# Optimization experiments

Hardware: AMD Instinct MI355X
Metric: run time of the kernel (lower is better)

The kernel has to match this reference:

```python
import jax, jax.numpy as jnp
import numpy as np

N_NODES = 100000
N_EDGES = 1600000
N_GRAPHS = 512
IN_F, H1, H2 = 128, 128, 256
N_GROUPS, N_FAM = 16, 10


def setup_inputs() -> dict:
    key = jax.random.key(0)
    ks = jax.random.split(key, 8)
    x = jax.random.normal(ks[0], (N_NODES, IN_F), dtype=jnp.float32)
    edge_index = jax.random.randint(ks[1], (2, N_EDGES), 0, N_NODES, dtype=jnp.int64)
    batch = jnp.sort(jax.random.randint(ks[2], (N_NODES,), 0, N_GRAPHS, dtype=jnp.int64))
    W1 = jax.random.normal(ks[3], (IN_F, H1), dtype=jnp.float32) / np.sqrt(IN_F)
    b1 = jnp.zeros((H1,), dtype=jnp.float32)
    W2 = jax.random.normal(ks[4], (H1, H2), dtype=jnp.float32) / np.sqrt(H1)
    b2 = jnp.zeros((H2,), dtype=jnp.float32)
    Wg = jax.random.normal(ks[5], (H2, N_GROUPS), dtype=jnp.float32) / np.sqrt(H2)
    bg = jnp.zeros((N_GROUPS,), dtype=jnp.float32)
    Wf = jax.random.normal(ks[6], (N_GROUPS, H2, N_FAM), dtype=jnp.float32) / np.sqrt(H2)
    bf = jnp.zeros((N_GROUPS, N_FAM), dtype=jnp.float32)
    return {"x": x, "edge_index": edge_index, "batch": batch,
            "W1": W1, "b1": b1, "W2": W2, "b2": b2,
            "Wg": Wg, "bg": bg, "Wf": Wf, "bf": bf}


def gcn_conv(x, W, b, src, dst, num_nodes):
    # PyG GCNConv: add self-loops, symmetric normalization, scatter-add aggregation.
    xw = x @ W  # [N, out]
    deg = jax.ops.segment_sum(jnp.ones((src.shape[0],), x.dtype), dst,
                              num_segments=num_nodes) + 1.0  # +1 self-loop
    dinv = jax.lax.rsqrt(deg)
    coef = dinv[src] * dinv[dst]            # [E]
    msg = xw[src] * coef[:, None]           # gather + scale (memory-bound)
    agg = jax.ops.segment_sum(msg, dst, num_segments=num_nodes)
    agg = agg + xw * (dinv * dinv)[:, None]  # self-loop contribution
    return agg + b


def reference(x, edge_index, batch, W1, b1, W2, b2, Wg, bg, Wf, bf):
    src, dst = edge_index[0], edge_index[1]
    h = jax.nn.relu(gcn_conv(x, W1, b1, src, dst, N_NODES))
    # dropout p=0.5 is identity in eval mode
    h = gcn_conv(h, W2, b2, src, dst, N_NODES)
    # global mean pool over graphs
    sums = jax.ops.segment_sum(h, batch, num_segments=N_GRAPHS)       # [G, H2]
    cnts = jax.ops.segment_sum(jnp.ones((N_NODES,), h.dtype), batch,
                               num_segments=N_GRAPHS)
    pooled = sums / jnp.maximum(cnts, 1.0)[:, None]
    group_logits = pooled @ Wg + bg                                   # [G, num_groups]
    family_logits = jnp.einsum('bd,gdf->gbf', pooled, Wf) + bf[:, None, :]
    return group_logits, family_logits
```

## Files before the change

kernel.cpp:

```cpp
#include <hip/hip_runtime.h>

#define NN 100000
#define NE 1600000
#define NGR 512
#define KF 128
#define H2F 256
#define NGRP 16
#define NFAM 10

#define CH 128
#define NCHUNK ((NN + CH - 1) / CH)
#define PT 6656
#define NT ((NE + PT - 1) / PT)

typedef __attribute__((ext_vector_type(8))) short short8;
typedef __attribute__((ext_vector_type(4))) float floatx4;

__device__ __forceinline__ unsigned short f2bf(float f) {
  unsigned u = __float_as_uint(f);
  unsigned r = (u + 0x7fff + ((u >> 16) & 1)) >> 16;
  return (unsigned short)r;
}
__device__ __forceinline__ float2 bf2f(unsigned u) {
  float2 r;
  r.x = __uint_as_float(u << 16);
  r.y = __uint_as_float(u & 0xffff0000u);
  return r;
}


__global__ __launch_bounds__(256) void k_phist(const int* __restrict__ ei,
                                               int* __restrict__ mat) {
  __shared__ int lh[NCHUNK];
  int t0 = blockIdx.x, tid = threadIdx.x;
  for (int g = tid; g < NCHUNK; g += 256) lh[g] = 0;
  __syncthreads();
  int base = t0 * PT;
  int nv = min(PT, NE - base);
  for (int i = tid; i < nv; i += 256) atomicAdd(&lh[ei[NE + base + i] >> 7], 1);
  __syncthreads();
  for (int g = tid; g < NCHUNK; g += 256) mat[t0 * NCHUNK + g] = lh[g];
}

__global__ __launch_bounds__(256) void k_colsum(const int* __restrict__ mat,
                                                int* __restrict__ tot) {
  int g = blockIdx.x * 4 + (threadIdx.x >> 6);
  if (g >= NCHUNK) return;
  int lane = threadIdx.x & 63;
  int s = 0;
  for (int t = lane; t < NT; t += 64) s += mat[t * NCHUNK + g];
#pragma unroll
  for (int off = 32; off > 0; off >>= 1) s += __shfl_down(s, off);
  if (lane == 0) tot[g] = s;
}

__global__ __launch_bounds__(256) void k_scantot(const int* __restrict__ tot,
                                                 int* __restrict__ cbase) {
  __shared__ int ssc[256];
  int tid = threadIdx.x;
  int v4[4]; int loc = 0;
#pragma unroll
  for (int j = 0; j < 4; ++j) {
    int idx = tid * 4 + j;
    v4[j] = (idx < NCHUNK) ? tot[idx] : 0;
    loc += v4[j];
  }
  ssc[tid] = loc;
  __syncthreads();
  for (int off = 1; off < 256; off <<= 1) {
    int val = (tid >= off) ? ssc[tid - off] : 0;
    __syncthreads();
    ssc[tid] += val;
    __syncthreads();
  }
  int excl = ssc[tid] - loc;
#pragma unroll
  for (int j = 0; j < 4; ++j) {
    int idx = tid * 4 + j;
    if (idx < NCHUNK) cbase[idx] = excl;
    excl += v4[j];
  }
  if (tid == 255) cbase[NCHUNK] = excl;
}

__global__ __launch_bounds__(256) void k_colfix(int* __restrict__ mat,
                                                const int* __restrict__ cbase) {
  int g = blockIdx.x * 4 + (threadIdx.x >> 6);
  if (g >= NCHUNK) return;
  int lane = threadIdx.x & 63;
  int v[4]; int loc = 0;
#pragma unroll
  for (int j = 0; j < 4; ++j) {
    int t = lane * 4 + j;
    v[j] = (t < NT) ? mat[t * NCHUNK + g] : 0;
    loc += v[j];
  }
  int incl = loc;
#pragma unroll
  for (int off = 1; off < 64; off <<= 1) {
    int o = __shfl_up(incl, off);
    if (lane >= off) incl += o;
  }
  int excl = incl - loc + cbase[g];
#pragma unroll
  for (int j = 0; j < 4; ++j) {
    int t = lane * 4 + j;
    if (t < NT) mat[t * NCHUNK + g] = excl;
    excl += v[j];
  }
}

__global__ __launch_bounds__(256) void k_pscatter(const int* __restrict__ ei,
                                                  const int* __restrict__ mat,
                                                  int2* __restrict__ erec) {
  __shared__ int2 stage[PT];
  __shared__ int lstart[NCHUNK];
  __shared__ int lrun[NCHUNK];
  __shared__ int loff[NCHUNK];
  __shared__ int ssc[256];
  int t0 = blockIdx.x, tid = threadIdx.x;
  for (int g = tid; g < NCHUNK; g += 256) lrun[g] = 0;
  __syncthreads();
  int base = t0 * PT;
  int nv = min(PT, NE - base);
  for (int i = tid; i < nv; i += 256) atomicAdd(&lrun[ei[NE + base + i] >> 7], 1);
  __syncthreads();
  int v4[4]; int loc = 0;
#pragma unroll
  for (int j = 0; j < 4; ++j) {
    int idx = tid * 4 + j;
    v4[j] = (idx < NCHUNK) ? lrun[idx] : 0;
    loc += v4[j];
  }
  ssc[tid] = loc;
  __syncthreads();
  for (int off = 1; off < 256; off <<= 1) {
    int val = (tid >= off) ? ssc[tid - off] : 0;
    __syncthreads();
    ssc[tid] += val;
    __syncthreads();
  }
  int excl = ssc[tid] - loc;
#pragma unroll
  for (int j = 0; j < 4; ++j) {
    int idx = tid * 4 + j;
    if (idx < NCHUNK) lstart[idx] = excl;
    excl += v4[j];
  }
  __syncthreads();
  for (int g = tid; g < NCHUNK; g += 256) {
    lrun[g] = lstart[g];
    loff[g] = mat[t0 * NCHUNK + g];
  }
  __syncthreads();
  for (int i = tid; i < nv; i += 256) {
    int s = ei[base + i], d = ei[NE + base + i];
    int pos = atomicAdd(&lrun[d >> 7], 1);
    stage[pos] = make_int2(s, d);
  }
  __syncthreads();
  for (int j = tid; j < nv; j += 256) {
    int2 r = stage[j];
    int g = r.y >> 7;
    erec[loff[g] + (j - lstart[g])] = r;
  }
}


__global__ __launch_bounds__(256) void k_sort(const int2* __restrict__ erec,
                                              const int* __restrict__ cbase,
                                              int* __restrict__ esrc,
                                              int* __restrict__ rowptr,
                                              float* __restrict__ dinv) {
  __shared__ int hist[CH];
  __shared__ int lrun[CH];
  __shared__ int sc[256];
  const int c = blockIdx.x, tid = threadIdx.x;
  const int e0 = cbase[c], e1 = cbase[c + 1];
  const int nv = e1 - e0;
  if (tid < CH) hist[tid] = 0;
  __syncthreads();
  for (int i = tid; i < nv; i += 256) atomicAdd(&hist[erec[e0 + i].y & (CH - 1)], 1);
  __syncthreads();
  int v = (tid < CH) ? hist[tid] : 0;
  sc[tid] = v;
  __syncthreads();
  for (int off = 1; off < 256; off <<= 1) {
    int val = (tid >= off) ? sc[tid - off] : 0;
    __syncthreads();
    sc[tid] += val;
    __syncthreads();
  }
  int excl = sc[tid] - v;
  if (tid < CH) lrun[tid] = excl;
  int node = c * CH + tid;
  if (tid < CH && node < NN) {
    rowptr[node] = e0 + excl;
    dinv[node] = rsqrtf((float)(v + 1));
  }
  if (c == NCHUNK - 1 && tid == CH - 1) rowptr[NN] = NE;
  if (c < NCHUNK - 1 && tid == 0) {  }
  __syncthreads();
  for (int i = tid; i < nv; i += 256) {
    int2 r = erec[e0 + i];
    int pos = atomicAdd(&lrun[r.y & (CH - 1)], 1);
    esrc[e0 + pos] = r.x;
  }
}


__global__ void k_prepB(const float* __restrict__ W, unsigned short* __restrict__ Bp,
                        int Ncol) {
  int idx = blockIdx.x * 256 + threadIdx.x;
  int total = 128 * Ncol;
  if (idx >= total) return;
  int NCH = Ncol >> 4;
  int j = idx & 7;
  int l = (idx >> 3) & 63;
  int rest = idx >> 9;
  int nc = rest % NCH;
  int kc = rest / NCH;
  int k = kc * 32 + (l >> 4) * 8 + j;
  int nn = nc * 16 + (l & 15);
  Bp[idx] = f2bf(W[k * Ncol + nn]);
}


__global__ __launch_bounds__(256) void k_gemm_mfma(const float* __restrict__ A,
                                                   const unsigned short* __restrict__ Bp,
                                                   unsigned short* __restrict__ C) {
  constexpr int K = 128;
  constexpr int N = KF;
  constexpr int NCH = N / 16;
  const int wv = blockIdx.x * 4 + (threadIdx.x >> 6);
  const int row0 = wv * 16;
  if (row0 >= NN) return;
  const int lane = threadIdx.x & 63;
  const int m = lane & 15;
  const int q = lane >> 4;

  floatx4 acc[NCH];
#pragma unroll
  for (int i = 0; i < NCH; ++i) acc[i] = (floatx4){0.f, 0.f, 0.f, 0.f};

  const int arow = row0 + m;
#pragma unroll
  for (int kc = 0; kc < 4; ++kc) {
    const float* ap = A + (size_t)arow * K + kc * 32 + q * 8;
    float4 f0 = *(const float4*)ap;
    float4 f1 = *(const float4*)(ap + 4);
    short8 af;
    af[0] = (short)f2bf(f0.x); af[1] = (short)f2bf(f0.y);
    af[2] = (short)f2bf(f0.z); af[3] = (short)f2bf(f0.w);
    af[4] = (short)f2bf(f1.x); af[5] = (short)f2bf(f1.y);
    af[6] = (short)f2bf(f1.z); af[7] = (short)f2bf(f1.w);
    const unsigned short* bp = Bp + (size_t)kc * NCH * 512;
#pragma unroll
    for (int nc = 0; nc < NCH; ++nc) {
      short8 bfr = *(const short8*)(bp + (size_t)nc * 512 + lane * 8);
      acc[nc] = __builtin_amdgcn_mfma_f32_16x16x32_bf16(af, bfr, acc[nc], 0, 0, 0);
    }
  }

#pragma unroll
  for (int nc = 0; nc < NCH; ++nc) {
#pragma unroll
    for (int r = 0; r < 4; ++r) {
      int row = row0 + q * 4 + r;
      C[(size_t)row * N + nc * 16 + m] = f2bf(acc[nc][r]);
    }
  }
}


template <bool RELU, bool BIAS>
__global__ __launch_bounds__(128) void k_agg(const unsigned* __restrict__ p,
                                             const float* __restrict__ bias,
                                             const int* __restrict__ rowptr,
                                             const int* __restrict__ esrc,
                                             const float* __restrict__ dinv,
                                             unsigned* __restrict__ out) {
  const int n = blockIdx.x * 2 + (threadIdx.x >> 6);
  const int t = threadIdx.x & 63;

  const float dn = dinv[n];
  const float dn2 = dn * dn;
  float2 f = bf2f(p[(size_t)n * 64 + t]);
  float ax = f.x * dn2, ay = f.y * dn2;

  const int r0 = rowptr[n];
  const int r1 = rowptr[n + 1];
  int i = r0;
  for (; i + 8 <= r1; i += 8) {
    int s0 = esrc[i], s1 = esrc[i + 1], s2 = esrc[i + 2], s3 = esrc[i + 3];
    int s4 = esrc[i + 4], s5 = esrc[i + 5], s6 = esrc[i + 6], s7 = esrc[i + 7];
    float c0 = dinv[s0] * dn, c1 = dinv[s1] * dn, c2 = dinv[s2] * dn, c3 = dinv[s3] * dn;
    float c4 = dinv[s4] * dn, c5 = dinv[s5] * dn, c6 = dinv[s6] * dn, c7 = dinv[s7] * dn;
    unsigned u0 = p[(size_t)s0 * 64 + t];
    unsigned u1 = p[(size_t)s1 * 64 + t];
    unsigned u2 = p[(size_t)s2 * 64 + t];
    unsigned u3 = p[(size_t)s3 * 64 + t];
    unsigned u4 = p[(size_t)s4 * 64 + t];
    unsigned u5 = p[(size_t)s5 * 64 + t];
    unsigned u6 = p[(size_t)s6 * 64 + t];
    unsigned u7 = p[(size_t)s7 * 64 + t];
    f = bf2f(u0); ax = fmaf(c0, f.x, ax); ay = fmaf(c0, f.y, ay);
    f = bf2f(u1); ax = fmaf(c1, f.x, ax); ay = fmaf(c1, f.y, ay);
    f = bf2f(u2); ax = fmaf(c2, f.x, ax); ay = fmaf(c2, f.y, ay);
    f = bf2f(u3); ax = fmaf(c3, f.x, ax); ay = fmaf(c3, f.y, ay);
    f = bf2f(u4); ax = fmaf(c4, f.x, ax); ay = fmaf(c4, f.y, ay);
    f = bf2f(u5); ax = fmaf(c5, f.x, ax); ay = fmaf(c5, f.y, ay);
    f = bf2f(u6); ax = fmaf(c6, f.x, ax); ay = fmaf(c6, f.y, ay);
    f = bf2f(u7); ax = fmaf(c7, f.x, ax); ay = fmaf(c7, f.y, ay);
  }
  for (; i + 4 <= r1; i += 4) {
    int s0 = esrc[i], s1 = esrc[i + 1], s2 = esrc[i + 2], s3 = esrc[i + 3];
    float c0 = dinv[s0] * dn, c1 = dinv[s1] * dn, c2 = dinv[s2] * dn, c3 = dinv[s3] * dn;
    unsigned u0 = p[(size_t)s0 * 64 + t];
    unsigned u1 = p[(size_t)s1 * 64 + t];
    unsigned u2 = p[(size_t)s2 * 64 + t];
    unsigned u3 = p[(size_t)s3 * 64 + t];
    f = bf2f(u0); ax = fmaf(c0, f.x, ax); ay = fmaf(c0, f.y, ay);
    f = bf2f(u1); ax = fmaf(c1, f.x, ax); ay = fmaf(c1, f.y, ay);
    f = bf2f(u2); ax = fmaf(c2, f.x, ax); ay = fmaf(c2, f.y, ay);
    f = bf2f(u3); ax = fmaf(c3, f.x, ax); ay = fmaf(c3, f.y, ay);
  }
  for (; i < r1; ++i) {
    int s = esrc[i];
    float c = dinv[s] * dn;
    f = bf2f(p[(size_t)s * 64 + t]);
    ax = fmaf(c, f.x, ax); ay = fmaf(c, f.y, ay);
  }

  if (BIAS) {
    float2 bb = ((const float2*)bias)[t];
    ax += bb.x; ay += bb.y;
  }
  if (RELU) { ax = fmaxf(ax, 0.f); ay = fmaxf(ay, 0.f); }
  out[(size_t)n * 64 + t] = (unsigned)f2bf(ax) | ((unsigned)f2bf(ay) << 16);
}


__global__ __launch_bounds__(256) void k_pool(const unsigned* __restrict__ p,
                                              const int* __restrict__ batch,
                                              float* __restrict__ pooled_raw) {
  int g = blockIdx.x;
  int t = threadIdx.x & 63;
  int wv = threadIdx.x >> 6;
  int lo = 0, hi = NN;
  while (lo < hi) { int mid = (lo + hi) >> 1; if (batch[mid] < g) lo = mid + 1; else hi = mid; }
  int start = lo;
  hi = NN;
  while (lo < hi) { int mid = (lo + hi) >> 1; if (batch[mid] < g + 1) lo = mid + 1; else hi = mid; }
  int end = lo;

  float sx = 0.f, sy = 0.f;
  int n = start + wv;
  for (; n + 12 < end; n += 16) {
    unsigned u0 = p[(size_t)n * 64 + t];
    unsigned u1 = p[(size_t)(n + 4) * 64 + t];
    unsigned u2 = p[(size_t)(n + 8) * 64 + t];
    unsigned u3 = p[(size_t)(n + 12) * 64 + t];
    float2 f0 = bf2f(u0), f1 = bf2f(u1), f2 = bf2f(u2), f3 = bf2f(u3);
    sx += (f0.x + f1.x) + (f2.x + f3.x);
    sy += (f0.y + f1.y) + (f2.y + f3.y);
  }
  for (; n < end; n += 4) {
    float2 f = bf2f(p[(size_t)n * 64 + t]);
    sx += f.x; sy += f.y;
  }

  __shared__ float sh[4][128];
  sh[wv][2 * t] = sx;
  sh[wv][2 * t + 1] = sy;
  __syncthreads();
  if (wv == 0) {
    float vx = sh[0][2 * t] + sh[1][2 * t] + sh[2][2 * t] + sh[3][2 * t];
    float vy = sh[0][2 * t + 1] + sh[1][2 * t + 1] + sh[2][2 * t + 1] + sh[3][2 * t + 1];
    float c = fmaxf((float)(end - start), 1.f);
    pooled_raw[g * KF + 2 * t] = vx / c;
    pooled_raw[g * KF + 2 * t + 1] = vy / c;
  }
}


__global__ __launch_bounds__(256) void k_heads(const float* __restrict__ praw,
                                               const float* __restrict__ W2,
                                               const float* __restrict__ b2,
                                               const float* __restrict__ Wg,
                                               const float* __restrict__ bg,
                                               const float* __restrict__ Wf,
                                               const float* __restrict__ bfb,
                                               float* __restrict__ out) {
  int b = blockIdx.x;
  int t = threadIdx.x;
  __shared__ float pr[KF];
  __shared__ float p[H2F];
  if (t < KF) pr[t] = praw[b * KF + t];
  __syncthreads();
  float acc = b2[t];
#pragma unroll 8
  for (int d = 0; d < KF; ++d) acc = fmaf(pr[d], W2[d * H2F + t], acc);
  p[t] = acc;
  __syncthreads();
  if (t < NGRP) {
    float a = bg[t];
    for (int d = 0; d < H2F; ++d) a = fmaf(p[d], Wg[d * NGRP + t], a);
    out[b * NGRP + t] = a;
  } else if (t >= 64 && t < 64 + NGRP * NFAM) {
    int u = t - 64;
    int g = u / NFAM;
    int ff = u % NFAM;
    float a = bfb[g * NFAM + ff];
    for (int d = 0; d < H2F; ++d) a = fmaf(p[d], Wf[(g * H2F + d) * NFAM + ff], a);
    out[NGR * NGRP + (size_t)g * NGR * NFAM + b * NFAM + ff] = a;
  }
}


extern "C" void kernel_launch(void* const* d_in, const int* in_sizes, int n_in,
                              void* d_out, int out_size, void* d_ws, size_t ws_size,
                              hipStream_t stream) {
  const float* x    = (const float*)d_in[0];
  const int*   ei   = (const int*)d_in[1];
  const int*   batch= (const int*)d_in[2];
  const float* W1   = (const float*)d_in[3];
  const float* b1   = (const float*)d_in[4];
  const float* W2   = (const float*)d_in[5];
  const float* b2   = (const float*)d_in[6];
  const float* Wg   = (const float*)d_in[7];
  const float* bg   = (const float*)d_in[8];
  const float* Wf   = (const float*)d_in[9];
  const float* bfb  = (const float*)d_in[10];
  float* out = (float*)d_out;

  char* w = (char*)d_ws;
  auto take = [&](size_t bytes) {
    char* p = w;
    w += (bytes + 255) & ~(size_t)255;
    return (void*)p;
  };
  int*   mat   = (int*)take((size_t)NT * NCHUNK * 4);
  int*   tot   = (int*)take((size_t)NCHUNK * 4);
  int*   cbase = (int*)take((size_t)(NCHUNK + 1) * 4);
  int2*  erec  = (int2*)take((size_t)NT * PT * 8);
  int*   esrc  = (int*)take((size_t)NE * 4);
  int*   rowptr= (int*)take((size_t)(NN + 1) * 4);
  float* dinv  = (float*)take((size_t)NN * 4);
  float* praw  = (float*)take((size_t)NGR * KF * 4);
  unsigned short* Bp1 = (unsigned short*)take((size_t)KF * KF * 2);
  unsigned* xw1 = (unsigned*)take((size_t)NN * KF * 2);
  unsigned* h1  = (unsigned*)take((size_t)NN * KF * 2);
  unsigned* agg2= (unsigned*)take((size_t)NN * KF * 2);

  k_phist<<<NT, 256, 0, stream>>>(ei, mat);
  k_colsum<<<(NCHUNK + 3) / 4, 256, 0, stream>>>(mat, tot);
  k_scantot<<<1, 256, 0, stream>>>(tot, cbase);
  k_colfix<<<(NCHUNK + 3) / 4, 256, 0, stream>>>(mat, cbase);
  k_pscatter<<<NT, 256, 0, stream>>>(ei, mat, erec);
  k_sort<<<NCHUNK, 256, 0, stream>>>(erec, cbase, esrc, rowptr, dinv);

  k_prepB<<<(KF * KF + 255) / 256, 256, 0, stream>>>(W1, Bp1, KF);
  k_gemm_mfma<<<1563, 256, 0, stream>>>(x, Bp1, (unsigned short*)xw1);

  k_agg<true, true><<<NN / 2, 128, 0, stream>>>(xw1, b1, rowptr, esrc, dinv, h1);
  k_agg<false, false><<<NN / 2, 128, 0, stream>>>(h1, nullptr, rowptr, esrc, dinv, agg2);

  k_pool<<<NGR, 256, 0, stream>>>(agg2, batch, praw);
  k_heads<<<NGR, 256, 0, stream>>>(praw, W2, b2, Wg, bg, Wf, bfb, out);
}
```

Measured before the change: 344.8 us.

## Prescale rows by dinv, pad CSR rows to 8, fuse pooling into second aggregation

Features are pre-multiplied by the source node's dinv in the GEMM epilogue and in layer 1's output. The edge loops then become plain sums without per-edge dinv gathers. CSR rows are padded to multiples of 8 with a dummy zero row, so neighbour indices load as int4 and the remainder loops disappear. Layer 2 aggregation atomically accumulates straight into per-graph pooled sums, and the mean division moves into the heads kernel. This removes the agg2 buffer and the separate pool pass, at the cost of float atomics, extra padded edges and memset/zero launches.

```diff
diff --git a/kernel.cpp b/kernel.cpp
--- a/kernel.cpp
+++ b/kernel.cpp
@@ -12,6 +12,7 @@
 #define NCHUNK ((NN + CH - 1) / CH)
 #define PT 6656
 #define NT ((NE + PT - 1) / PT)
+#define CSLACK 1024
 
 typedef __attribute__((ext_vector_type(8))) short short8;
 typedef __attribute__((ext_vector_type(4))) float floatx4;
@@ -178,12 +179,15 @@
   const int c = blockIdx.x, tid = threadIdx.x;
   const int e0 = cbase[c], e1 = cbase[c + 1];
   const int nv = e1 - e0;
+  const int pb = ((e0 + 7) & ~7) + c * CSLACK;
+  const int pe = ((e1 + 7) & ~7) + (c + 1) * CSLACK;
   if (tid < CH) hist[tid] = 0;
   __syncthreads();
   for (int i = tid; i < nv; i += 256) atomicAdd(&hist[erec[e0 + i].y & (CH - 1)], 1);
   __syncthreads();
-  int v = (tid < CH) ? hist[tid] : 0;
-  sc[tid] = v;
+  int deg = (tid < CH) ? hist[tid] : 0;
+  int pd = (deg + 7) & ~7;
+  sc[tid] = pd;
   __syncthreads();
   for (int off = 1; off < 256; off <<= 1) {
     int val = (tid >= off) ? sc[tid - off] : 0;
@@ -191,21 +195,31 @@
     sc[tid] += val;
     __syncthreads();
   }
-  int excl = sc[tid] - v;
-  if (tid < CH) lrun[tid] = excl;
+  int excl = sc[tid] - pd;
   int node = c * CH + tid;
-  if (tid < CH && node < NN) {
-    rowptr[node] = e0 + excl;
-    dinv[node] = rsqrtf((float)(v + 1));
-  }
-  if (c == NCHUNK - 1 && tid == CH - 1) rowptr[NN] = NE;
-  if (c < NCHUNK - 1 && tid == 0) {  }
+  if (tid < CH) {
+    lrun[tid] = excl;
+    if (node < NN) {
+      rowptr[node] = pb + excl;
+      dinv[node] = rsqrtf((float)(deg + 1));
+    }
+    if (node == NN) rowptr[NN] = pb + excl;
+  }
+  __syncthreads();
+  for (int i = pb + tid; i < pe; i += 256) esrc[i] = NN;
   __syncthreads();
   for (int i = tid; i < nv; i += 256) {
     int2 r = erec[e0 + i];
     int pos = atomicAdd(&lrun[r.y & (CH - 1)], 1);
-    esrc[e0 + pos] = r.x;
-  }
+    esrc[pb + pos] = r.x;
+  }
+}
+
+
+__global__ void k_zero(unsigned* __restrict__ a, unsigned* __restrict__ b) {
+  int t = threadIdx.x;
+  a[(size_t)NN * 64 + t] = 0;
+  b[(size_t)NN * 64 + t] = 0;
 }
 
 
@@ -228,6 +242,7 @@
 
 __global__ __launch_bounds__(256) void k_gemm_mfma(const float* __restrict__ A,
                                                    const unsigned short* __restrict__ Bp,
+                                                   const float* __restrict__ dinv,
                                                    unsigned short* __restrict__ C) {
   constexpr int K = 128;
   constexpr int N = KF;
@@ -262,129 +277,109 @@
     }
   }
 
+  float ds[4];
+#pragma unroll
+  for (int r = 0; r < 4; ++r) ds[r] = dinv[row0 + q * 4 + r];
 #pragma unroll
   for (int nc = 0; nc < NCH; ++nc) {
 #pragma unroll
     for (int r = 0; r < 4; ++r) {
       int row = row0 + q * 4 + r;
-      C[(size_t)row * N + nc * 16 + m] = f2bf(acc[nc][r]);
+      C[(size_t)row * N + nc * 16 + m] = f2bf(acc[nc][r] * ds[r]);
     }
   }
 }
 
 
-template <bool RELU, bool BIAS>
-__global__ __launch_bounds__(128) void k_agg(const unsigned* __restrict__ p,
-                                             const float* __restrict__ bias,
-                                             const int* __restrict__ rowptr,
-                                             const int* __restrict__ esrc,
-                                             const float* __restrict__ dinv,
-                                             unsigned* __restrict__ out) {
+__global__ __launch_bounds__(128) void k_agg1(const unsigned* __restrict__ p,
+                                              const float* __restrict__ bias,
+                                              const int* __restrict__ rowptr,
+                                              const int* __restrict__ esrc,
+                                              const float* __restrict__ dinv,
+                                              unsigned* __restrict__ out) {
   const int n = blockIdx.x * 2 + (threadIdx.x >> 6);
   const int t = threadIdx.x & 63;
 
-  const float dn = dinv[n];
-  const float dn2 = dn * dn;
   float2 f = bf2f(p[(size_t)n * 64 + t]);
-  float ax = f.x * dn2, ay = f.y * dn2;
+  float ax = f.x, ay = f.y;
 
   const int r0 = rowptr[n];
   const int r1 = rowptr[n + 1];
-  int i = r0;
-  for (; i + 8 <= r1; i += 8) {
-    int s0 = esrc[i], s1 = esrc[i + 1], s2 = esrc[i + 2], s3 = esrc[i + 3];
-    int s4 = esrc[i + 4], s5 = esrc[i + 5], s6 = esrc[i + 6], s7 = esrc[i + 7];
-    float c0 = dinv[s0] * dn, c1 = dinv[s1] * dn, c2 = dinv[s2] * dn, c3 = dinv[s3] * dn;
-    float c4 = dinv[s4] * dn, c5 = dinv[s5] * dn, c6 = dinv[s6] * dn, c7 = dinv[s7] * dn;
-    unsigned u0 = p[(size_t)s0 * 64 + t];
-    unsigned u1 = p[(size_t)s1 * 64 + t];
-    unsigned u2 = p[(size_t)s2 * 64 + t];
-    unsigned u3 = p[(size_t)s3 * 64 + t];
-    unsigned u4 = p[(size_t)s4 * 64 + t];
-    unsigned u5 = p[(size_t)s5 * 64 + t];
-    unsigned u6 = p[(size_t)s6 * 64 + t];
-    unsigned u7 = p[(size_t)s7 * 64 + t];
-    f = bf2f(u0); ax = fmaf(c0, f.x, ax); ay = fmaf(c0, f.y, ay);
-    f = bf2f(u1); ax = fmaf(c1, f.x, ax); ay = fmaf(c1, f.y, ay);
-    f = bf2f(u2); ax = fmaf(c2, f.x, ax); ay = fmaf(c2, f.y, ay);
-    f = bf2f(u3); ax = fmaf(c3, f.x, ax); ay = fmaf(c3, f.y, ay);
-    f = bf2f(u4); ax = fmaf(c4, f.x, ax); ay = fmaf(c4, f.y, ay);
-    f = bf2f(u5); ax = fmaf(c5, f.x, ax); ay = fmaf(c5, f.y, ay);
-    f = bf2f(u6); ax = fmaf(c6, f.x, ax); ay = fmaf(c6, f.y, ay);
-    f = bf2f(u7); ax = fmaf(c7, f.x, ax); ay = fmaf(c7, f.y, ay);
-  }
-  for (; i + 4 <= r1; i += 4) {
-    int s0 = esrc[i], s1 = esrc[i + 1], s2 = esrc[i + 2], s3 = esrc[i + 3];
-    float c0 = dinv[s0] * dn, c1 = dinv[s1] * dn, c2 = dinv[s2] * dn, c3 = dinv[s3] * dn;
-    unsigned u0 = p[(size_t)s0 * 64 + t];
-    unsigned u1 = p[(size_t)s1 * 64 + t];
-    unsigned u2 = p[(size_t)s2 * 64 + t];
-    unsigned u3 = p[(size_t)s3 * 64 + t];
-    f = bf2f(u0); ax = fmaf(c0, f.x, ax); ay = fmaf(c0, f.y, ay);
-    f = bf2f(u1); ax = fmaf(c1, f.x, ax); ay = fmaf(c1, f.y, ay);
-    f = bf2f(u2); ax = fmaf(c2, f.x, ax); ay = fmaf(c2, f.y, ay);
-    f = bf2f(u3); ax = fmaf(c3, f.x, ax); ay = fmaf(c3, f.y, ay);
-  }
-  for (; i < r1; ++i) {
-    int s = esrc[i];
-    float c = dinv[s] * dn;
-    f = bf2f(p[(size_t)s * 64 + t]);
-    ax = fmaf(c, f.x, ax); ay = fmaf(c, f.y, ay);
-  }
-
-  if (BIAS) {
-    float2 bb = ((const float2*)bias)[t];
-    ax += bb.x; ay += bb.y;
-  }
-  if (RELU) { ax = fmaxf(ax, 0.f); ay = fmaxf(ay, 0.f); }
+  for (int i = r0; i < r1; i += 8) {
+    int4 ea = *(const int4*)(esrc + i);
+    int4 eb = *(const int4*)(esrc + i + 4);
+    unsigned u0 = p[(size_t)ea.x * 64 + t];
+    unsigned u1 = p[(size_t)ea.y * 64 + t];
+    unsigned u2 = p[(size_t)ea.z * 64 + t];
+    unsigned u3 = p[(size_t)ea.w * 64 + t];
+    unsigned u4 = p[(size_t)eb.x * 64 + t];
+    unsigned u5 = p[(size_t)eb.y * 64 + t];
+    unsigned u6 = p[(size_t)eb.z * 64 + t];
+    unsigned u7 = p[(size_t)eb.w * 64 + t];
+    f = bf2f(u0); ax += f.x; ay += f.y;
+    f = bf2f(u1); ax += f.x; ay += f.y;
+    f = bf2f(u2); ax += f.x; ay += f.y;
+    f = bf2f(u3); ax += f.x; ay += f.y;
+    f = bf2f(u4); ax += f.x; ay += f.y;
+    f = bf2f(u5); ax += f.x; ay += f.y;
+    f = bf2f(u6); ax += f.x; ay += f.y;
+    f = bf2f(u7); ax += f.x; ay += f.y;
+  }
+
+  const float dn = dinv[n];
+  float2 bb = ((const float2*)bias)[t];
+  ax = fmaf(dn, ax, bb.x);
+  ay = fmaf(dn, ay, bb.y);
+  ax = fmaxf(ax, 0.f) * dn;
+  ay = fmaxf(ay, 0.f) * dn;
   out[(size_t)n * 64 + t] = (unsigned)f2bf(ax) | ((unsigned)f2bf(ay) << 16);
 }
 
 
-__global__ __launch_bounds__(256) void k_pool(const unsigned* __restrict__ p,
+__global__ __launch_bounds__(128) void k_agg2(const unsigned* __restrict__ p,
+                                              const int* __restrict__ rowptr,
+                                              const int* __restrict__ esrc,
+                                              const float* __restrict__ dinv,
                                               const int* __restrict__ batch,
-                                              float* __restrict__ pooled_raw) {
-  int g = blockIdx.x;
-  int t = threadIdx.x & 63;
-  int wv = threadIdx.x >> 6;
-  int lo = 0, hi = NN;
-  while (lo < hi) { int mid = (lo + hi) >> 1; if (batch[mid] < g) lo = mid + 1; else hi = mid; }
-  int start = lo;
-  hi = NN;
-  while (lo < hi) { int mid = (lo + hi) >> 1; if (batch[mid] < g + 1) lo = mid + 1; else hi = mid; }
-  int end = lo;
-
-  float sx = 0.f, sy = 0.f;
-  int n = start + wv;
-  for (; n + 12 < end; n += 16) {
-    unsigned u0 = p[(size_t)n * 64 + t];
-    unsigned u1 = p[(size_t)(n + 4) * 64 + t];
-    unsigned u2 = p[(size_t)(n + 8) * 64 + t];
-    unsigned u3 = p[(size_t)(n + 12) * 64 + t];
-    float2 f0 = bf2f(u0), f1 = bf2f(u1), f2 = bf2f(u2), f3 = bf2f(u3);
-    sx += (f0.x + f1.x) + (f2.x + f3.x);
-    sy += (f0.y + f1.y) + (f2.y + f3.y);
-  }
-  for (; n < end; n += 4) {
-    float2 f = bf2f(p[(size_t)n * 64 + t]);
-    sx += f.x; sy += f.y;
-  }
-
-  __shared__ float sh[4][128];
-  sh[wv][2 * t] = sx;
-  sh[wv][2 * t + 1] = sy;
-  __syncthreads();
-  if (wv == 0) {
-    float vx = sh[0][2 * t] + sh[1][2 * t] + sh[2][2 * t] + sh[3][2 * t];
-    float vy = sh[0][2 * t + 1] + sh[1][2 * t + 1] + sh[2][2 * t + 1] + sh[3][2 * t + 1];
-    float c = fmaxf((float)(end - start), 1.f);
-    pooled_raw[g * KF + 2 * t] = vx / c;
-    pooled_raw[g * KF + 2 * t + 1] = vy / c;
-  }
+                                              float* __restrict__ praw) {
+  const int n = blockIdx.x * 2 + (threadIdx.x >> 6);
+  const int t = threadIdx.x & 63;
+
+  float2 f = bf2f(p[(size_t)n * 64 + t]);
+  float ax = f.x, ay = f.y;
+
+  const int r0 = rowptr[n];
+  const int r1 = rowptr[n + 1];
+  for (int i = r0; i < r1; i += 8) {
+    int4 ea = *(const int4*)(esrc + i);
+    int4 eb = *(const int4*)(esrc + i + 4);
+    unsigned u0 = p[(size_t)ea.x * 64 + t];
+    unsigned u1 = p[(size_t)ea.y * 64 + t];
+    unsigned u2 = p[(size_t)ea.z * 64 + t];
+    unsigned u3 = p[(size_t)ea.w * 64 + t];
+    unsigned u4 = p[(size_t)eb.x * 64 + t];
+    unsigned u5 = p[(size_t)eb.y * 64 + t];
+    unsigned u6 = p[(size_t)eb.z * 64 + t];
+    unsigned u7 = p[(size_t)eb.w * 64 + t];
+    f = bf2f(u0); ax += f.x; ay += f.y;
+    f = bf2f(u1); ax += f.x; ay += f.y;
+    f = bf2f(u2); ax += f.x; ay += f.y;
+    f = bf2f(u3); ax += f.x; ay += f.y;
+    f = bf2f(u4); ax += f.x; ay += f.y;
+    f = bf2f(u5); ax += f.x; ay += f.y;
+    f = bf2f(u6); ax += f.x; ay += f.y;
+    f = bf2f(u7); ax += f.x; ay += f.y;
+  }
+
+  const float dn = dinv[n];
+  const int g = batch[n];
+  atomicAdd(&praw[g * KF + 2 * t], dn * ax);
+  atomicAdd(&praw[g * KF + 2 * t + 1], dn * ay);
 }
 
 
 __global__ __launch_bounds__(256) void k_heads(const float* __restrict__ praw,
+                                               const int* __restrict__ batch,
                                                const float* __restrict__ W2,
                                                const float* __restrict__ b2,
                                                const float* __restrict__ Wg,
@@ -396,7 +391,16 @@
   int t = threadIdx.x;
   __shared__ float pr[KF];
   __shared__ float p[H2F];
-  if (t < KF) pr[t] = praw[b * KF + t];
+  __shared__ int bnd[2];
+  if (t < 2) {
+    int target = b + t;
+    int lo = 0, hi = NN;
+    while (lo < hi) { int mid = (lo + hi) >> 1; if (batch[mid] < target) lo = mid + 1; else hi = mid; }
+    bnd[t] = lo;
+  }
+  __syncthreads();
+  float cg = fmaxf((float)(bnd[1] - bnd[0]), 1.f);
+  if (t < KF) pr[t] = praw[b * KF + t] / cg;
   __syncthreads();
   float acc = b2[t];
 #pragma unroll 8
@@ -444,14 +448,15 @@
   int*   tot   = (int*)take((size_t)NCHUNK * 4);
   int*   cbase = (int*)take((size_t)(NCHUNK + 1) * 4);
   int2*  erec  = (int2*)take((size_t)NT * PT * 8);
-  int*   esrc  = (int*)take((size_t)NE * 4);
+  int*   esrc  = (int*)take(((size_t)NE + (size_t)NCHUNK * CSLACK + 16) * 4);
   int*   rowptr= (int*)take((size_t)(NN + 1) * 4);
   float* dinv  = (float*)take((size_t)NN * 4);
   float* praw  = (float*)take((size_t)NGR * KF * 4);
   unsigned short* Bp1 = (unsigned short*)take((size_t)KF * KF * 2);
-  unsigned* xw1 = (unsigned*)take((size_t)NN * KF * 2);
-  unsigned* h1  = (unsigned*)take((size_t)NN * KF * 2);
-  unsigned* agg2= (unsigned*)take((size_t)NN * KF * 2);
+  unsigned* xw1 = (unsigned*)take((size_t)(NN + 1) * KF * 2);
+  unsigned* h1  = (unsigned*)take((size_t)(NN + 1) * KF * 2);
+
+  hipMemsetAsync(praw, 0, (size_t)NGR * KF * 4, stream);
 
   k_phist<<<NT, 256, 0, stream>>>(ei, mat);
   k_colsum<<<(NCHUNK + 3) / 4, 256, 0, stream>>>(mat, tot);
@@ -460,12 +465,12 @@
   k_pscatter<<<NT, 256, 0, stream>>>(ei, mat, erec);
   k_sort<<<NCHUNK, 256, 0, stream>>>(erec, cbase, esrc, rowptr, dinv);
 
+  k_zero<<<1, 64, 0, stream>>>(xw1, h1);
   k_prepB<<<(KF * KF + 255) / 256, 256, 0, stream>>>(W1, Bp1, KF);
-  k_gemm_mfma<<<1563, 256, 0, stream>>>(x, Bp1, (unsigned short*)xw1);
-
-  k_agg<true, true><<<NN / 2, 128, 0, stream>>>(xw1, b1, rowptr, esrc, dinv, h1);
-  k_agg<false, false><<<NN / 2, 128, 0, stream>>>(h1, nullptr, rowptr, esrc, dinv, agg2);
-
-  k_pool<<<NGR, 256, 0, stream>>>(agg2, batch, praw);
-  k_heads<<<NGR, 256, 0, stream>>>(praw, W2, b2, Wg, bg, Wf, bfb, out);
-}
+  k_gemm_mfma<<<1563, 256, 0, stream>>>(x, Bp1, dinv, (unsigned short*)xw1);
+
+  k_agg1<<<NN / 2, 128, 0, stream>>>(xw1, b1, rowptr, esrc, dinv, h1);
+  k_agg2<<<NN / 2, 128, 0, stream>>>(h1, rowptr, esrc, dinv, batch, praw);
+
+  k_heads<<<NGR, 256, 0, stream>>>(praw, batch, W2, b2, Wg, bg, Wf, bfb, out);
+}
```

Measured after the change: 925.7 us. 2.68x slower.

## Fold symmetric GCN normalization into source prescale and destination postscale

Applied to the files above, without the earlier changes.

Source rows are prescaled by dinv once, in the GEMM epilogue for layer 1 and in the layer-1 aggregation output for layer 2. Each edge then needs only a plain add, with no per-edge dinv gather or multiply, and the destination scaling is applied once per node at the end. This removes a random 4-byte gather and an FMA per edge per lane. It adds one extra bf16 rounding of the prescaled values, and it relies on rowptr[NN] being set from the padded chunk, which changes how the last row pointer is written.

```diff
diff --git a/kernel.cpp b/kernel.cpp
--- a/kernel.cpp
+++ b/kernel.cpp
@@ -182,8 +182,8 @@
   __syncthreads();
   for (int i = tid; i < nv; i += 256) atomicAdd(&hist[erec[e0 + i].y & (CH - 1)], 1);
   __syncthreads();
-  int v = (tid < CH) ? hist[tid] : 0;
-  sc[tid] = v;
+  int deg = (tid < CH) ? hist[tid] : 0;
+  sc[tid] = deg;
   __syncthreads();
   for (int off = 1; off < 256; off <<= 1) {
     int val = (tid >= off) ? sc[tid - off] : 0;
@@ -191,15 +191,17 @@
     sc[tid] += val;
     __syncthreads();
   }
-  int excl = sc[tid] - v;
-  if (tid < CH) lrun[tid] = excl;
+  int excl = sc[tid] - deg;
   int node = c * CH + tid;
-  if (tid < CH && node < NN) {
-    rowptr[node] = e0 + excl;
-    dinv[node] = rsqrtf((float)(v + 1));
-  }
-  if (c == NCHUNK - 1 && tid == CH - 1) rowptr[NN] = NE;
-  if (c < NCHUNK - 1 && tid == 0) {  }
+  if (tid < CH) {
+    lrun[tid] = excl;
+    if (node < NN) {
+      rowptr[node] = e0 + excl;
+      dinv[node] = rsqrtf((float)(deg + 1));
+    } else if (node == NN) {
+      rowptr[NN] = e0 + excl;
+    }
+  }
   __syncthreads();
   for (int i = tid; i < nv; i += 256) {
     int2 r = erec[e0 + i];
@@ -228,6 +230,7 @@
 
 __global__ __launch_bounds__(256) void k_gemm_mfma(const float* __restrict__ A,
                                                    const unsigned short* __restrict__ Bp,
+                                                   const float* __restrict__ dinv,
                                                    unsigned short* __restrict__ C) {
   constexpr int K = 128;
   constexpr int N = KF;
@@ -262,18 +265,21 @@
     }
   }
 
+  float ds[4];
+#pragma unroll
+  for (int r = 0; r < 4; ++r) ds[r] = dinv[row0 + q * 4 + r];
 #pragma unroll
   for (int nc = 0; nc < NCH; ++nc) {
 #pragma unroll
     for (int r = 0; r < 4; ++r) {
       int row = row0 + q * 4 + r;
-      C[(size_t)row * N + nc * 16 + m] = f2bf(acc[nc][r]);
+      C[(size_t)row * N + nc * 16 + m] = f2bf(acc[nc][r] * ds[r]);
     }
   }
 }
 
 
-template <bool RELU, bool BIAS>
+template <bool FIRST>
 __global__ __launch_bounds__(128) void k_agg(const unsigned* __restrict__ p,
                                              const float* __restrict__ bias,
                                              const int* __restrict__ rowptr,
@@ -283,10 +289,8 @@
   const int n = blockIdx.x * 2 + (threadIdx.x >> 6);
   const int t = threadIdx.x & 63;
 
-  const float dn = dinv[n];
-  const float dn2 = dn * dn;
   float2 f = bf2f(p[(size_t)n * 64 + t]);
-  float ax = f.x * dn2, ay = f.y * dn2;
+  float ax = f.x, ay = f.y;
 
   const int r0 = rowptr[n];
   const int r1 = rowptr[n + 1];
@@ -294,8 +298,6 @@
   for (; i + 8 <= r1; i += 8) {
     int s0 = esrc[i], s1 = esrc[i + 1], s2 = esrc[i + 2], s3 = esrc[i + 3];
     int s4 = esrc[i + 4], s5 = esrc[i + 5], s6 = esrc[i + 6], s7 = esrc[i + 7];
-    float c0 = dinv[s0] * dn, c1 = dinv[s1] * dn, c2 = dinv[s2] * dn, c3 = dinv[s3] * dn;
-    float c4 = dinv[s4] * dn, c5 = dinv[s5] * dn, c6 = dinv[s6] * dn, c7 = dinv[s7] * dn;
     unsigned u0 = p[(size_t)s0 * 64 + t];
     unsigned u1 = p[(size_t)s1 * 64 + t];
     unsigned u2 = p[(size_t)s2 * 64 + t];
@@ -304,39 +306,43 @@
     unsigned u5 = p[(size_t)s5 * 64 + t];
     unsigned u6 = p[(size_t)s6 * 64 + t];
     unsigned u7 = p[(size_t)s7 * 64 + t];
-    f = bf2f(u0); ax = fmaf(c0, f.x, ax); ay = fmaf(c0, f.y, ay);
-    f = bf2f(u1); ax = fmaf(c1, f.x, ax); ay = fmaf(c1, f.y, ay);
-    f = bf2f(u2); ax = fmaf(c2, f.x, ax); ay = fmaf(c2, f.y, ay);
-    f = bf2f(u3); ax = fmaf(c3, f.x, ax); ay = fmaf(c3, f.y, ay);
-    f = bf2f(u4); ax = fmaf(c4, f.x, ax); ay = fmaf(c4, f.y, ay);
-    f = bf2f(u5); ax = fmaf(c5, f.x, ax); ay = fmaf(c5, f.y, ay);
-    f = bf2f(u6); ax = fmaf(c6, f.x, ax); ay = fmaf(c6, f.y, ay);
-    f = bf2f(u7); ax = fmaf(c7, f.x, ax); ay = fmaf(c7, f.y, ay);
+    f = bf2f(u0); ax += f.x; ay += f.y;
+    f = bf2f(u1); ax += f.x; ay += f.y;
+    f = bf2f(u2); ax += f.x; ay += f.y;
+    f = bf2f(u3); ax += f.x; ay += f.y;
+    f = bf2f(u4); ax += f.x; ay += f.y;
+    f = bf2f(u5); ax += f.x; ay += f.y;
+    f = bf2f(u6); ax += f.x; ay += f.y;
+    f = bf2f(u7); ax += f.x; ay += f.y;
   }
   for (; i + 4 <= r1; i += 4) {
     int s0 = esrc[i], s1 = esrc[i + 1], s2 = esrc[i + 2], s3 = esrc[i + 3];
-    float c0 = dinv[s0] * dn, c1 = dinv[s1] * dn, c2 = dinv[s2] * dn, c3 = dinv[s3] * dn;
     unsigned u0 = p[(size_t)s0 * 64 + t];
     unsigned u1 = p[(size_t)s1 * 64 + t];
     unsigned u2 = p[(size_t)s2 * 64 + t];
     unsigned u3 = p[(size_t)s3 * 64 + t];
-    f = bf2f(u0); ax = fmaf(c0, f.x, ax); ay = fmaf(c0, f.y, ay);
-    f = bf2f(u1); ax = fmaf(c1, f.x, ax); ay = fmaf(c1, f.y, ay);
-    f = bf2f(u2); ax = fmaf(c2, f.x, ax); ay = fmaf(c2, f.y, ay);
-    f = bf2f(u3); ax = fmaf(c3, f.x, ax); ay = fmaf(c3, f.y, ay);
+    f = bf2f(u0); ax += f.x; ay += f.y;
+    f = bf2f(u1); ax += f.x; ay += f.y;
+    f = bf2f(u2); ax += f.x; ay += f.y;
+    f = bf2f(u3); ax += f.x; ay += f.y;
   }
   for (; i < r1; ++i) {
     int s = esrc[i];
-    float c = dinv[s] * dn;
     f = bf2f(p[(size_t)s * 64 + t]);
-    ax = fmaf(c, f.x, ax); ay = fmaf(c, f.y, ay);
-  }
-
-  if (BIAS) {
+    ax += f.x; ay += f.y;
+  }
+
+  const float dn = dinv[n];
+  if (FIRST) {
     float2 bb = ((const float2*)bias)[t];
-    ax += bb.x; ay += bb.y;
-  }
-  if (RELU) { ax = fmaxf(ax, 0.f); ay = fmaxf(ay, 0.f); }
+    ax = fmaf(dn, ax, bb.x);
+    ay = fmaf(dn, ay, bb.y);
+    ax = fmaxf(ax, 0.f) * dn;
+    ay = fmaxf(ay, 0.f) * dn;
+  } else {
+    ax *= dn;
+    ay *= dn;
+  }
   out[(size_t)n * 64 + t] = (unsigned)f2bf(ax) | ((unsigned)f2bf(ay) << 16);
 }
 
@@ -461,10 +467,10 @@
   k_sort<<<NCHUNK, 256, 0, stream>>>(erec, cbase, esrc, rowptr, dinv);
 
   k_prepB<<<(KF * KF + 255) / 256, 256, 0, stream>>>(W1, Bp1, KF);
-  k_gemm_mfma<<<1563, 256, 0, stream>>>(x, Bp1, (unsigned short*)xw1);
-
-  k_agg<true, true><<<NN / 2, 128, 0, stream>>>(xw1, b1, rowptr, esrc, dinv, h1);
-  k_agg<false, false><<<NN / 2, 128, 0, stream>>>(h1, nullptr, rowptr, esrc, dinv, agg2);
+  k_gemm_mfma<<<1563, 256, 0, stream>>>(x, Bp1, dinv, (unsigned short*)xw1);
+
+  k_agg<true><<<NN / 2, 128, 0, stream>>>(xw1, b1, rowptr, esrc, dinv, h1);
+  k_agg<false><<<NN / 2, 128, 0, stream>>>(h1, nullptr, rowptr, esrc, dinv, agg2);
 
   k_pool<<<NGR, 256, 0, stream>>>(agg2, batch, praw);
   k_heads<<<NGR, 256, 0, stream>>>(praw, W2, b2, Wg, bg, Wf, bfb, out);
```

After: 347.9 us. About the same (+0.9%).
